# Optimization experiments

Hardware: AMD Instinct MI355X
Metric: run time of the kernel (lower is better)

The kernel has to match this reference:

```python
import jax, jax.numpy as jnp
import numpy as np

B, T, D, H, O = 64, 512, 1024, 128, 128


def setup_inputs() -> dict:
    key = jax.random.key(0)
    ks = jax.random.split(key, 9)
    s1 = 1.0 / np.sqrt(H)
    s2 = 1.0 / np.sqrt(O)
    return {
        "feats": jax.random.normal(ks[0], (B, T, D), dtype=jnp.float32),
        "W_ih1": jax.random.uniform(ks[1], (4 * H, D), jnp.float32, -s1, s1),
        "W_hh1": jax.random.uniform(ks[2], (4 * H, H), jnp.float32, -s1, s1),
        "b_ih1": jax.random.uniform(ks[3], (4 * H,), jnp.float32, -s1, s1),
        "b_hh1": jax.random.uniform(ks[4], (4 * H,), jnp.float32, -s1, s1),
        "W_ih2": jax.random.uniform(ks[5], (4 * O, H), jnp.float32, -s2, s2),
        "W_hh2": jax.random.uniform(ks[6], (4 * O, O), jnp.float32, -s2, s2),
        "b_ih2": jax.random.uniform(ks[7], (4 * O,), jnp.float32, -s2, s2),
        "b_hh2": jax.random.uniform(ks[8], (4 * O,), jnp.float32, -s2, s2),
    }


def _gates(pre, c):
    # PyTorch LSTMCell gate order: i, f, g, o
    i, f, g, o = jnp.split(pre, 4, axis=-1)
    c_new = jax.nn.sigmoid(f) * c + jax.nn.sigmoid(i) * jnp.tanh(g)
    h_new = jax.nn.sigmoid(o) * jnp.tanh(c_new)
    return h_new, c_new


def reference(feats, W_ih1, W_hh1, b_ih1, b_hh1, W_ih2, W_hh2, b_ih2, b_hh2):
    b = feats.shape[0]
    # Precompute input contributions for layer 1 across all timesteps: [T, B, 4H]
    x1 = jnp.einsum("btd,gd->tbg", feats, W_ih1) + b_ih1 + b_hh1
    b2 = b_ih2 + b_hh2

    def step(carry, xg):
        h1, c1, h2, c2 = carry
        h1, c1 = _gates(xg + h1 @ W_hh1.T, c1)
        h2, c2 = _gates(h1 @ W_ih2.T + b2 + h2 @ W_hh2.T, c2)
        return (h1, c1, h2, c2), h2

    init = (
        jnp.zeros((b, W_hh1.shape[1]), feats.dtype),
        jnp.zeros((b, W_hh1.shape[1]), feats.dtype),
        jnp.zeros((b, W_hh2.shape[1]), feats.dtype),
        jnp.zeros((b, W_hh2.shape[1]), feats.dtype),
    )
    _, stream = jax.lax.scan(step, init, x1)  # stream: [T, B, O]
    return jnp.transpose(stream, (1, 0, 2))  # [B, T, O]
```

## Files before the change

kernel.cpp:

```cpp
#include <hip/hip_runtime.h>

using u16 = unsigned short;
using u32 = unsigned int;

typedef short bf16x8 __attribute__((ext_vector_type(8)));
typedef float f32x4  __attribute__((ext_vector_type(4)));

__device__ __forceinline__ float bf2f(u16 u) {
    union { u32 u; float f; } v; v.u = ((u32)u) << 16; return v.f;
}
__device__ __forceinline__ u16 f2bf(float f) {
    union { float f; u32 u; } v; v.f = f;
    u32 r = v.u + 0x7FFFu + ((v.u >> 16) & 1u);
    return (u16)(r >> 16);
}
__device__ __forceinline__ float fsig(float x)  { return 1.f / (1.f + __expf(-x)); }
__device__ __forceinline__ float ftanh(float x) { return 1.f - 2.f / (__expf(2.f * x) + 1.f); }

__device__ __forceinline__ uint4 pack8(const u16 h[8]) {
    uint4 u;
    u.x = (u32)h[0] | ((u32)h[1] << 16);
    u.y = (u32)h[2] | ((u32)h[3] << 16);
    u.z = (u32)h[4] | ((u32)h[5] << 16);
    u.w = (u32)h[6] | ((u32)h[7] << 16);
    return u;
}
__device__ __forceinline__ bf16x8 cvt8f(const float* p) {
    bf16x8 r;
    #pragma unroll
    for (int j = 0; j < 8; ++j) r[j] = (short)f2bf(p[j]);
    return r;
}

__device__ __forceinline__ u32 aload(const u32* p) {
    return __hip_atomic_load((u32*)p, __ATOMIC_RELAXED, __HIP_MEMORY_SCOPE_AGENT);
}
__device__ __forceinline__ void astore(u32* p, u32 v) {
    __hip_atomic_store(p, v, __ATOMIC_RELAXED, __HIP_MEMORY_SCOPE_AGENT);
}
__device__ __forceinline__ bf16x8 afrag(const u16* base16) {
    union { u32 w[4]; bf16x8 f; } u;
    const u32* p = (const u32*)base16;
    #pragma unroll
    for (int i = 0; i < 4; ++i) u.w[i] = aload(p + i);
    return u.f;
}

__global__ __launch_bounds__(256) void x1_gemm(
    const float* __restrict__ feats, const float* __restrict__ Wih1,
    const float* __restrict__ bih1, const float* __restrict__ bhh1,
    float* __restrict__ x1p)
{
    __shared__ uint4 a_hi[128 * 8];
    __shared__ uint4 a_lo[128 * 8];
    __shared__ uint4 b_hi[128 * 8];
    __shared__ uint4 b_lo[128 * 8];
    const int tid  = threadIdx.x;
    const int lane = tid & 63, wave = tid >> 6;
    const int m0 = blockIdx.x * 128, n0 = blockIdx.y * 128;
    const int wm = (wave >> 1) * 64, wn = (wave & 1) * 64;
    const int lr = lane & 15, lk = lane >> 4;

    f32x4 acc[4][4] = {};

    for (int kt = 0; kt < 1024; kt += 64) {
        __syncthreads();
        #pragma unroll
        for (int it = 0; it < 4; ++it) {
            int idx = tid + it * 256;
            int row = idx >> 3, c8 = idx & 7;
            int sw  = (row << 3) | (c8 ^ (row & 7));
            size_t offA = (size_t)(m0 + row) * 1024 + kt + c8 * 8;
            size_t offB = (size_t)(n0 + row) * 1024 + kt + c8 * 8;
            {
                const float* p = feats + offA;
                float4 v0 = *reinterpret_cast<const float4*>(p);
                float4 v1 = *reinterpret_cast<const float4*>(p + 4);
                float av[8] = {v0.x, v0.y, v0.z, v0.w, v1.x, v1.y, v1.z, v1.w};
                u16 h[8], l[8];
                #pragma unroll
                for (int j = 0; j < 8; ++j) {
                    h[j] = f2bf(av[j]);
                    l[j] = f2bf(av[j] - bf2f(h[j]));
                }
                a_hi[sw] = pack8(h);
                a_lo[sw] = pack8(l);
            }
            {
                const float* p = Wih1 + offB;
                float4 v0 = *reinterpret_cast<const float4*>(p);
                float4 v1 = *reinterpret_cast<const float4*>(p + 4);
                float bv[8] = {v0.x, v0.y, v0.z, v0.w, v1.x, v1.y, v1.z, v1.w};
                u16 h[8], l[8];
                #pragma unroll
                for (int j = 0; j < 8; ++j) {
                    h[j] = f2bf(bv[j]);
                    l[j] = f2bf(bv[j] - bf2f(h[j]));
                }
                b_hi[sw] = pack8(h);
                b_lo[sw] = pack8(l);
            }
        }
        __syncthreads();
        for (int s = 0; s < 3; ++s) {
            const uint4* ab = (s == 2) ? a_lo : a_hi;
            const uint4* bb = (s == 1) ? b_lo : b_hi;
            #pragma unroll
            for (int kc = 0; kc < 2; ++kc) {
                bf16x8 af[4], bfr[4];
                #pragma unroll
                for (int i = 0; i < 4; ++i) {
                    int row = wm + i * 16 + lr;
                    af[i] = *reinterpret_cast<const bf16x8*>(&ab[(row << 3) | ((kc * 4 + lk) ^ (row & 7))]);
                }
                #pragma unroll
                for (int j = 0; j < 4; ++j) {
                    int row = wn + j * 16 + lr;
                    bfr[j] = *reinterpret_cast<const bf16x8*>(&bb[(row << 3) | ((kc * 4 + lk) ^ (row & 7))]);
                }
                #pragma unroll
                for (int i = 0; i < 4; ++i)
                    #pragma unroll
                    for (int j = 0; j < 4; ++j)
                        acc[i][j] = __builtin_amdgcn_mfma_f32_16x16x32_bf16(af[i], bfr[j], acc[i][j], 0, 0, 0);
            }
        }
    }
    #pragma unroll
    for (int j = 0; j < 4; ++j) {
        int n = n0 + wn + j * 16 + lr;
        float bias = bih1[n] + bhh1[n];
        #pragma unroll
        for (int i = 0; i < 4; ++i) {
            #pragma unroll
            for (int q = 0; q < 4; ++q) {
                int m = m0 + wm + i * 16 + lk * 4 + q;
                int b = m >> 9, t = m & 511;
                size_t o = ((size_t)(t * 64 + b)) * 512 + n;
                x1p[o] = acc[i][j][q] + bias;
            }
        }
    }
}

__global__ __launch_bounds__(512, 2) void lstm_scan3(
    const float* __restrict__ Whh1, const float* __restrict__ Wih2,
    const float* __restrict__ Whh2, const float* __restrict__ bih2,
    const float* __restrict__ bhh2, const float* __restrict__ x1p,
    u16* __restrict__ h1s,
    u32* __restrict__ prodf,
    u32* __restrict__ consf,
    float* __restrict__ out)
{
    const int tid = threadIdx.x;
    const int wv = tid >> 6, ln = tid & 63;
    const int lr = ln & 15, lk = ln >> 4;
    const int blk = blockIdx.x;
    const bool is1 = (blk < 4);
    const int bg = is1 ? blk : blk - 4;

    u32* prodp = prodf + bg;
    u32* consp = consf + bg;

    if (is1) {
        bf16x8 wf[4][4];
        #pragma unroll
        for (int G = 0; G < 4; ++G) {
            int n = G * 128 + wv * 16 + lr;
            #pragma unroll
            for (int kc = 0; kc < 4; ++kc)
                wf[G][kc] = cvt8f(Whh1 + n * 128 + kc * 32 + lk * 8);
        }
        const int rowoff = (bg * 16 + lk * 4) * 512 + wv * 16 + lr;
        float xn[4][4], xc[4][4];
        #pragma unroll
        for (int G = 0; G < 4; ++G)
            #pragma unroll
            for (int q = 0; q < 4; ++q)
                xn[G][q] = x1p[rowoff + q * 512 + G * 128];
        float c[4] = {0.f, 0.f, 0.f, 0.f};
        u32 consc = 0;

        for (int r = 0; r < 512; ++r) {
            #pragma unroll
            for (int G = 0; G < 4; ++G)
                #pragma unroll
                for (int q = 0; q < 4; ++q) xc[G][q] = xn[G][q];

            bf16x8 a[4];
            if (r == 0) {
                bf16x8 zz = {0, 0, 0, 0, 0, 0, 0, 0};
                #pragma unroll
                for (int kc = 0; kc < 4; ++kc) a[kc] = zz;
            } else {
                const u16* sb = h1s + (size_t)(((r - 1) % 3) * 4 + bg) * 2048;
                #pragma unroll
                for (int kc = 0; kc < 4; ++kc)
                    a[kc] = afrag(sb + lr * 128 + kc * 32 + lk * 8);
            }
            if (r + 1 < 512) {
                const float* xb = x1p + (size_t)(r + 1) * 32768 + rowoff;
                #pragma unroll
                for (int G = 0; G < 4; ++G)
                    #pragma unroll
                    for (int q = 0; q < 4; ++q)
                        xn[G][q] = xb[q * 512 + G * 128];
            }
            f32x4 acc[4] = {};
            #pragma unroll
            for (int kc = 0; kc < 4; ++kc)
                #pragma unroll
                for (int G = 0; G < 4; ++G)
                    acc[G] = __builtin_amdgcn_mfma_f32_16x16x32_bf16(a[kc], wf[G][kc], acc[G], 0, 0, 0);

            if (r >= 3) {
                u32 need = (u32)(r - 2);
                while (consc < need) {
                    consc = aload(consp);
                    if (consc < need) __builtin_amdgcn_s_sleep(2);
                }
            }
            u32* ob = (u32*)(h1s + (size_t)((r % 3) * 4 + bg) * 2048);
            #pragma unroll
            for (int q = 0; q < 4; ++q) {
                float pi = acc[0][q] + xc[0][q];
                float pf = acc[1][q] + xc[1][q];
                float pg = acc[2][q] + xc[2][q];
                float po = acc[3][q] + xc[3][q];
                float ig = fsig(pi), fg = fsig(pf), gg = ftanh(pg), og = fsig(po);
                c[q] = fg * c[q] + ig * gg;
                float h = og * ftanh(c[q]);
                u32 mine = f2bf(h);
                u32 part = (u32)__shfl_xor((int)mine, 1, 64);
                if (!(lr & 1))
                    astore(ob + (lk * 4 + q) * 64 + ((wv * 16 + lr) >> 1), mine | (part << 16));
            }
            __syncthreads();
            if (tid == 0) astore(prodp, (u32)(r + 1));
        }
    } else {
        bf16x8 wa[4][4], wb[4][4];
        float b2v[4];
        #pragma unroll
        for (int G = 0; G < 4; ++G) {
            int n = G * 128 + wv * 16 + lr;
            #pragma unroll
            for (int kc = 0; kc < 4; ++kc) {
                wa[G][kc] = cvt8f(Wih2 + n * 128 + kc * 32 + lk * 8);
                wb[G][kc] = cvt8f(Whh2 + n * 128 + kc * 32 + lk * 8);
            }
            b2v[G] = bih2[n] + bhh2[n];
        }
        u32 prodc = 0;
        while (prodc < 1u) {
            prodc = aload(prodp);
            if (prodc < 1u) __builtin_amdgcn_s_sleep(2);
        }
        bf16x8 a1c[4], a1n[4];
        {
            const u16* sb = h1s + (size_t)bg * 2048;
            #pragma unroll
            for (int kc = 0; kc < 4; ++kc)
                a1c[kc] = afrag(sb + lr * 128 + kc * 32 + lk * 8);
        }
        const float* selfout = out + (size_t)(bg * 16 + lr) * 512 * 128;
        float c[4] = {0.f, 0.f, 0.f, 0.f};

        for (int r = 0; r < 512; ++r) {
            bf16x8 a2[4];
            if (r == 0) {
                bf16x8 zz = {0, 0, 0, 0, 0, 0, 0, 0};
                #pragma unroll
                for (int kc = 0; kc < 4; ++kc) a2[kc] = zz;
            } else {
                const float* hb = selfout + (size_t)(r - 1) * 128;
                #pragma unroll
                for (int kc = 0; kc < 4; ++kc)
                    a2[kc] = cvt8f(hb + kc * 32 + lk * 8);
            }
            f32x4 acc[4] = {};
            #pragma unroll
            for (int kc = 0; kc < 4; ++kc)
                #pragma unroll
                for (int G = 0; G < 4; ++G)
                    acc[G] = __builtin_amdgcn_mfma_f32_16x16x32_bf16(a1c[kc], wa[G][kc], acc[G], 0, 0, 0);
            #pragma unroll
            for (int kc = 0; kc < 4; ++kc)
                #pragma unroll
                for (int G = 0; G < 4; ++G)
                    acc[G] = __builtin_amdgcn_mfma_f32_16x16x32_bf16(a2[kc], wb[G][kc], acc[G], 0, 0, 0);

            if (r + 1 < 512) {
                u32 need = (u32)(r + 2);
                while (prodc < need) {
                    prodc = aload(prodp);
                    if (prodc < need) __builtin_amdgcn_s_sleep(2);
                }
                const u16* sb = h1s + (size_t)(((r + 1) % 3) * 4 + bg) * 2048;
                #pragma unroll
                for (int kc = 0; kc < 4; ++kc)
                    a1n[kc] = afrag(sb + lr * 128 + kc * 32 + lk * 8);
            }

            float* orow = out + ((size_t)(bg * 16 + lk * 4) * 512 + r) * 128 + wv * 16 + lr;
            #pragma unroll
            for (int q = 0; q < 4; ++q) {
                float pi = acc[0][q] + b2v[0];
                float pf = acc[1][q] + b2v[1];
                float pg = acc[2][q] + b2v[2];
                float po = acc[3][q] + b2v[3];
                float ig = fsig(pi), fg = fsig(pf), gg = ftanh(pg), og = fsig(po);
                c[q] = fg * c[q] + ig * gg;
                float h = og * ftanh(c[q]);
                orow[(size_t)q * 512 * 128] = h;
            }
            __syncthreads();
            if (tid == 0) astore(consp, (u32)(r + 1));
            if (r + 1 < 512) {
                #pragma unroll
                for (int kc = 0; kc < 4; ++kc) a1c[kc] = a1n[kc];
            }
        }
    }
}

extern "C" void kernel_launch(void* const* d_in, const int* in_sizes, int n_in,
                              void* d_out, int out_size, void* d_ws, size_t ws_size,
                              hipStream_t stream)
{
    const float* feats = (const float*)d_in[0];
    const float* Wih1  = (const float*)d_in[1];
    const float* Whh1  = (const float*)d_in[2];
    const float* bih1  = (const float*)d_in[3];
    const float* bhh1  = (const float*)d_in[4];
    const float* Wih2  = (const float*)d_in[5];
    const float* Whh2  = (const float*)d_in[6];
    const float* bih2  = (const float*)d_in[7];
    const float* bhh2  = (const float*)d_in[8];
    float* out = (float*)d_out;

    const size_t x1b = (size_t)32768 * 512 * 4;
    if (ws_size < x1b + 49152 + 128) return;

    char* ws   = (char*)d_ws;
    float* x1p = (float*)ws;
    u16* h1s   = (u16*)(ws + x1b);
    u32* prodf = (u32*)(ws + x1b + 49152);
    u32* consf = (u32*)(ws + x1b + 49152 + 64);

    hipMemsetAsync(ws + x1b + 49152, 0, 128, stream);
    x1_gemm<<<dim3(256, 4), 256, 0, stream>>>(feats, Wih1, bih1, bhh1, x1p);
    lstm_scan3<<<8, 512, 0, stream>>>(Whh1, Wih2, Whh2, bih2, bhh2,
                                      x1p, h1s, prodf, consf, out);
    (void)in_sizes; (void)n_in; (void)out_size;
}
```

Before: 3.439 ms.

## Fuse both LSTM layers into one block per batch group with LDS state

Replaces the producer/consumer pair of blocks, which synchronised through global atomic flags and a global h1 ring buffer, with a single block per batch group. That block computes layer 1 for step r+1 and layer 2 for step r in the same iteration, skewed by one step. Hidden states are double-buffered in swizzled LDS, and x1 rows are prefetched into LDS with global_load_lds. W_hh2 is pre-converted to bf16 in a separate kernel and streamed from global memory each step instead of held in registers. This removes the cross-block spin-wait latency and the global round trips for h1 and h2, but now runs only 4 blocks, each doing both layers' work serially and reloading W_hh2 every step.

```diff
diff --git a/kernel.cpp b/kernel.cpp
--- a/kernel.cpp
+++ b/kernel.cpp
@@ -32,18 +32,17 @@
     return r;
 }
 
-__device__ __forceinline__ u32 aload(const u32* p) {
-    return __hip_atomic_load((u32*)p, __ATOMIC_RELAXED, __HIP_MEMORY_SCOPE_AGENT);
-}
-__device__ __forceinline__ void astore(u32* p, u32 v) {
-    __hip_atomic_store(p, v, __ATOMIC_RELAXED, __HIP_MEMORY_SCOPE_AGENT);
-}
-__device__ __forceinline__ bf16x8 afrag(const u16* base16) {
-    union { u32 w[4]; bf16x8 f; } u;
-    const u32* p = (const u32*)base16;
-    #pragma unroll
-    for (int i = 0; i < 4; ++i) u.w[i] = aload(p + i);
-    return u.f;
+__device__ __forceinline__ void gld_lds16(const void* g, void* l) {
+    __builtin_amdgcn_global_load_lds(
+        (const __attribute__((address_space(1))) unsigned int*)g,
+        (__attribute__((address_space(3))) unsigned int*)l, 16, 0, 0);
+}
+
+__global__ __launch_bounds__(512) void wconv(const float* __restrict__ Whh2,
+                                             u16* __restrict__ wbg)
+{
+    int i = blockIdx.x * 512 + threadIdx.x;
+    wbg[i] = f2bf(Whh2[i]);
 }
 
 __global__ __launch_bounds__(256) void x1_gemm(
@@ -143,184 +142,143 @@
     }
 }
 
-__global__ __launch_bounds__(512, 2) void lstm_scan3(
+__global__ __launch_bounds__(512) void lstm_fused(
     const float* __restrict__ Whh1, const float* __restrict__ Wih2,
-    const float* __restrict__ Whh2, const float* __restrict__ bih2,
+    const u16*  __restrict__ wbg,   const float* __restrict__ bih2,
     const float* __restrict__ bhh2, const float* __restrict__ x1p,
-    u16* __restrict__ h1s,
-    u32* __restrict__ prodf,
-    u32* __restrict__ consf,
     float* __restrict__ out)
 {
+    __shared__ __align__(16) char smem[81920];
+    char* xb  = smem;
+    char* h1b = smem + 65536;
+    char* h2b = smem + 73728;
+
     const int tid = threadIdx.x;
     const int wv = tid >> 6, ln = tid & 63;
     const int lr = ln & 15, lk = ln >> 4;
-    const int blk = blockIdx.x;
-    const bool is1 = (blk < 4);
-    const int bg = is1 ? blk : blk - 4;
-
-    u32* prodp = prodf + bg;
-    u32* consp = consf + bg;
-
-    if (is1) {
-        bf16x8 wf[4][4];
-        #pragma unroll
-        for (int G = 0; G < 4; ++G) {
-            int n = G * 128 + wv * 16 + lr;
-            #pragma unroll
-            for (int kc = 0; kc < 4; ++kc)
-                wf[G][kc] = cvt8f(Whh1 + n * 128 + kc * 32 + lk * 8);
-        }
-        const int rowoff = (bg * 16 + lk * 4) * 512 + wv * 16 + lr;
-        float xn[4][4], xc[4][4];
-        #pragma unroll
-        for (int G = 0; G < 4; ++G)
-            #pragma unroll
-            for (int q = 0; q < 4; ++q)
-                xn[G][q] = x1p[rowoff + q * 512 + G * 128];
-        float c[4] = {0.f, 0.f, 0.f, 0.f};
-        u32 consc = 0;
-
-        for (int r = 0; r < 512; ++r) {
+    const int bg = blockIdx.x;
+    const int colP = wv * 16 + lr;
+    const int rowB = lk * 4;
+
+    bf16x8 wf[4][4], wa[4][4];
+    float b2v[4];
+    #pragma unroll
+    for (int G = 0; G < 4; ++G) {
+        int n = G * 128 + colP;
+        #pragma unroll
+        for (int kc = 0; kc < 4; ++kc) {
+            wf[G][kc] = cvt8f(Whh1 + n * 128 + kc * 32 + lk * 8);
+            wa[G][kc] = cvt8f(Wih2 + n * 128 + kc * 32 + lk * 8);
+        }
+        b2v[G] = bih2[n] + bhh2[n];
+    }
+
+    for (int i = tid; i < 1024; i += 512) ((u32*)(h2b + 4096))[i] = 0;
+
+    {
+        const float* s = x1p + (size_t)(bg * 16) * 512 + wv * 1024 + ln * 4;
+        char* d = xb + wv * 4096;
+        #pragma unroll
+        for (int i = 0; i < 4; ++i) gld_lds16(s + i * 256, d + i * 1024);
+    }
+    __syncthreads();
+
+    float c1[4] = {0.f, 0.f, 0.f, 0.f}, c2[4] = {0.f, 0.f, 0.f, 0.f};
+
+    #pragma unroll
+    for (int q = 0; q < 4; ++q) {
+        const float* xr = (const float*)(xb + (rowB + q) * 2048);
+        float pi = xr[0 * 128 + colP];
+        float pf = xr[1 * 128 + colP];
+        float pg = xr[2 * 128 + colP];
+        float po = xr[3 * 128 + colP];
+        float ig = fsig(pi), fg = fsig(pf), gg = ftanh(pg), og = fsig(po);
+        c1[q] = fg * c1[q] + ig * gg;
+        float h = og * ftanh(c1[q]);
+        int row = rowB + q;
+        *(u16*)(h1b + row * 256 + ((((colP >> 3) ^ row) & 15) << 4) + (colP & 7) * 2)
+            = f2bf(h);
+    }
+    {
+        const float* s = x1p + (size_t)(64 + bg * 16) * 512 + wv * 1024 + ln * 4;
+        char* d = xb + 32768 + wv * 4096;
+        #pragma unroll
+        for (int i = 0; i < 4; ++i) gld_lds16(s + i * 256, d + i * 1024);
+    }
+    __syncthreads();
+
+    for (int r = 0; r < 512; ++r) {
+        const char* h1rd = h1b + ((r & 1) << 12);
+        char*       h1wr = h1b + (((r + 1) & 1) << 12);
+        const char* h2rd = h2b + (((r + 1) & 1) << 12);
+        char*       h2wr = h2b + ((r & 1) << 12);
+        const char* xrd  = xb  + (((r + 1) & 1) << 15);
+
+        bf16x8 a1[4];
+        #pragma unroll
+        for (int kc = 0; kc < 4; ++kc)
+            a1[kc] = *(const bf16x8*)(h1rd + lr * 256 + ((((kc * 4 + lk) ^ lr) & 15) << 4));
+
+        if (r + 2 < 512) {
+            const float* s = x1p + (size_t)((r + 2) * 64 + bg * 16) * 512 + wv * 1024 + ln * 4;
+            char* d = xb + ((r & 1) << 15) + wv * 4096;
+            #pragma unroll
+            for (int i = 0; i < 4; ++i) gld_lds16(s + i * 256, d + i * 1024);
+        }
+
+        f32x4 acc2[4] = {}, acch[4] = {};
+        #pragma unroll
+        for (int kc = 0; kc < 4; ++kc)
             #pragma unroll
             for (int G = 0; G < 4; ++G)
-                #pragma unroll
-                for (int q = 0; q < 4; ++q) xc[G][q] = xn[G][q];
-
-            bf16x8 a[4];
-            if (r == 0) {
-                bf16x8 zz = {0, 0, 0, 0, 0, 0, 0, 0};
-                #pragma unroll
-                for (int kc = 0; kc < 4; ++kc) a[kc] = zz;
-            } else {
-                const u16* sb = h1s + (size_t)(((r - 1) % 3) * 4 + bg) * 2048;
-                #pragma unroll
-                for (int kc = 0; kc < 4; ++kc)
-                    a[kc] = afrag(sb + lr * 128 + kc * 32 + lk * 8);
-            }
-            if (r + 1 < 512) {
-                const float* xb = x1p + (size_t)(r + 1) * 32768 + rowoff;
-                #pragma unroll
-                for (int G = 0; G < 4; ++G)
-                    #pragma unroll
-                    for (int q = 0; q < 4; ++q)
-                        xn[G][q] = xb[q * 512 + G * 128];
-            }
-            f32x4 acc[4] = {};
-            #pragma unroll
-            for (int kc = 0; kc < 4; ++kc)
-                #pragma unroll
-                for (int G = 0; G < 4; ++G)
-                    acc[G] = __builtin_amdgcn_mfma_f32_16x16x32_bf16(a[kc], wf[G][kc], acc[G], 0, 0, 0);
-
-            if (r >= 3) {
-                u32 need = (u32)(r - 2);
-                while (consc < need) {
-                    consc = aload(consp);
-                    if (consc < need) __builtin_amdgcn_s_sleep(2);
-                }
-            }
-            u32* ob = (u32*)(h1s + (size_t)((r % 3) * 4 + bg) * 2048);
+                acc2[G] = __builtin_amdgcn_mfma_f32_16x16x32_bf16(a1[kc], wa[G][kc], acc2[G], 0, 0, 0);
+        #pragma unroll
+        for (int kc = 0; kc < 4; ++kc) {
+            bf16x8 a2 = *(const bf16x8*)(h2rd + lr * 256 + ((((kc * 4 + lk) ^ lr) & 15) << 4));
+            #pragma unroll
+            for (int G = 0; G < 4; ++G) {
+                bf16x8 wbf = *(const bf16x8*)(wbg + (size_t)(G * 128 + colP) * 128 + kc * 32 + lk * 8);
+                acc2[G] = __builtin_amdgcn_mfma_f32_16x16x32_bf16(a2, wbf, acc2[G], 0, 0, 0);
+            }
+        }
+        #pragma unroll
+        for (int kc = 0; kc < 4; ++kc)
+            #pragma unroll
+            for (int G = 0; G < 4; ++G)
+                acch[G] = __builtin_amdgcn_mfma_f32_16x16x32_bf16(a1[kc], wf[G][kc], acch[G], 0, 0, 0);
+
+        float* orow = out + ((size_t)(bg * 16 + rowB) * 512 + r) * 128 + colP;
+        #pragma unroll
+        for (int q = 0; q < 4; ++q) {
+            float pi = acc2[0][q] + b2v[0];
+            float pf = acc2[1][q] + b2v[1];
+            float pg = acc2[2][q] + b2v[2];
+            float po = acc2[3][q] + b2v[3];
+            float ig = fsig(pi), fg = fsig(pf), gg = ftanh(pg), og = fsig(po);
+            c2[q] = fg * c2[q] + ig * gg;
+            float h = og * ftanh(c2[q]);
+            int row = rowB + q;
+            *(u16*)(h2wr + row * 256 + ((((colP >> 3) ^ row) & 15) << 4) + (colP & 7) * 2)
+                = f2bf(h);
+            orow[(size_t)q * 512 * 128] = h;
+        }
+        if (r + 1 < 512) {
             #pragma unroll
             for (int q = 0; q < 4; ++q) {
-                float pi = acc[0][q] + xc[0][q];
-                float pf = acc[1][q] + xc[1][q];
-                float pg = acc[2][q] + xc[2][q];
-                float po = acc[3][q] + xc[3][q];
+                const float* xr = (const float*)(xrd + (rowB + q) * 2048);
+                float pi = acch[0][q] + xr[0 * 128 + colP];
+                float pf = acch[1][q] + xr[1 * 128 + colP];
+                float pg = acch[2][q] + xr[2 * 128 + colP];
+                float po = acch[3][q] + xr[3 * 128 + colP];
                 float ig = fsig(pi), fg = fsig(pf), gg = ftanh(pg), og = fsig(po);
-                c[q] = fg * c[q] + ig * gg;
-                float h = og * ftanh(c[q]);
-                u32 mine = f2bf(h);
-                u32 part = (u32)__shfl_xor((int)mine, 1, 64);
-                if (!(lr & 1))
-                    astore(ob + (lk * 4 + q) * 64 + ((wv * 16 + lr) >> 1), mine | (part << 16));
-            }
-            __syncthreads();
-            if (tid == 0) astore(prodp, (u32)(r + 1));
-        }
-    } else {
-        bf16x8 wa[4][4], wb[4][4];
-        float b2v[4];
-        #pragma unroll
-        for (int G = 0; G < 4; ++G) {
-            int n = G * 128 + wv * 16 + lr;
-            #pragma unroll
-            for (int kc = 0; kc < 4; ++kc) {
-                wa[G][kc] = cvt8f(Wih2 + n * 128 + kc * 32 + lk * 8);
-                wb[G][kc] = cvt8f(Whh2 + n * 128 + kc * 32 + lk * 8);
-            }
-            b2v[G] = bih2[n] + bhh2[n];
-        }
-        u32 prodc = 0;
-        while (prodc < 1u) {
-            prodc = aload(prodp);
-            if (prodc < 1u) __builtin_amdgcn_s_sleep(2);
-        }
-        bf16x8 a1c[4], a1n[4];
-        {
-            const u16* sb = h1s + (size_t)bg * 2048;
-            #pragma unroll
-            for (int kc = 0; kc < 4; ++kc)
-                a1c[kc] = afrag(sb + lr * 128 + kc * 32 + lk * 8);
-        }
-        const float* selfout = out + (size_t)(bg * 16 + lr) * 512 * 128;
-        float c[4] = {0.f, 0.f, 0.f, 0.f};
-
-        for (int r = 0; r < 512; ++r) {
-            bf16x8 a2[4];
-            if (r == 0) {
-                bf16x8 zz = {0, 0, 0, 0, 0, 0, 0, 0};
-                #pragma unroll
-                for (int kc = 0; kc < 4; ++kc) a2[kc] = zz;
-            } else {
-                const float* hb = selfout + (size_t)(r - 1) * 128;
-                #pragma unroll
-                for (int kc = 0; kc < 4; ++kc)
-                    a2[kc] = cvt8f(hb + kc * 32 + lk * 8);
-            }
-            f32x4 acc[4] = {};
-            #pragma unroll
-            for (int kc = 0; kc < 4; ++kc)
-                #pragma unroll
-                for (int G = 0; G < 4; ++G)
-                    acc[G] = __builtin_amdgcn_mfma_f32_16x16x32_bf16(a1c[kc], wa[G][kc], acc[G], 0, 0, 0);
-            #pragma unroll
-            for (int kc = 0; kc < 4; ++kc)
-                #pragma unroll
-                for (int G = 0; G < 4; ++G)
-                    acc[G] = __builtin_amdgcn_mfma_f32_16x16x32_bf16(a2[kc], wb[G][kc], acc[G], 0, 0, 0);
-
-            if (r + 1 < 512) {
-                u32 need = (u32)(r + 2);
-                while (prodc < need) {
-                    prodc = aload(prodp);
-                    if (prodc < need) __builtin_amdgcn_s_sleep(2);
-                }
-                const u16* sb = h1s + (size_t)(((r + 1) % 3) * 4 + bg) * 2048;
-                #pragma unroll
-                for (int kc = 0; kc < 4; ++kc)
-                    a1n[kc] = afrag(sb + lr * 128 + kc * 32 + lk * 8);
-            }
-
-            float* orow = out + ((size_t)(bg * 16 + lk * 4) * 512 + r) * 128 + wv * 16 + lr;
-            #pragma unroll
-            for (int q = 0; q < 4; ++q) {
-                float pi = acc[0][q] + b2v[0];
-                float pf = acc[1][q] + b2v[1];
-                float pg = acc[2][q] + b2v[2];
-                float po = acc[3][q] + b2v[3];
-                float ig = fsig(pi), fg = fsig(pf), gg = ftanh(pg), og = fsig(po);
-                c[q] = fg * c[q] + ig * gg;
-                float h = og * ftanh(c[q]);
-                orow[(size_t)q * 512 * 128] = h;
-            }
-            __syncthreads();
-            if (tid == 0) astore(consp, (u32)(r + 1));
-            if (r + 1 < 512) {
-                #pragma unroll
-                for (int kc = 0; kc < 4; ++kc) a1c[kc] = a1n[kc];
-            }
-        }
+                c1[q] = fg * c1[q] + ig * gg;
+                float h = og * ftanh(c1[q]);
+                int row = rowB + q;
+                *(u16*)(h1wr + row * 256 + ((((colP >> 3) ^ row) & 15) << 4) + (colP & 7) * 2)
+                    = f2bf(h);
+            }
+        }
+        __syncthreads();
     }
 }
 
@@ -340,17 +298,14 @@
     float* out = (float*)d_out;
 
     const size_t x1b = (size_t)32768 * 512 * 4;
-    if (ws_size < x1b + 49152 + 128) return;
+    if (ws_size < x1b + 131072) return;
 
     char* ws   = (char*)d_ws;
     float* x1p = (float*)ws;
-    u16* h1s   = (u16*)(ws + x1b);
-    u32* prodf = (u32*)(ws + x1b + 49152);
-    u32* consf = (u32*)(ws + x1b + 49152 + 64);
-
-    hipMemsetAsync(ws + x1b + 49152, 0, 128, stream);
+    u16*  wbg  = (u16*)(ws + x1b);
+
+    wconv<<<128, 512, 0, stream>>>(Whh2, wbg);
     x1_gemm<<<dim3(256, 4), 256, 0, stream>>>(feats, Wih1, bih1, bhh1, x1p);
-    lstm_scan3<<<8, 512, 0, stream>>>(Whh1, Wih2, Whh2, bih2, bhh2,
-                                      x1p, h1s, prodf, consf, out);
+    lstm_fused<<<4, 512, 0, stream>>>(Whh1, Wih2, wbg, bih2, bhh2, x1p, out);
     (void)in_sizes; (void)n_in; (void)out_size;
 }
```

Result: faster. 2.901 ms (-15.7%).
